# Kernel tuning notes

Hardware: AMD Instinct MI355X
Metric: run time of the kernel (lower is better)

The kernel has to match this reference:

```python
import math
import jax, jax.numpy as jnp
import numpy as np


def _coeffs(alpha, delta, theta, gamma_real, gamma_imag):
    # alpha, delta: (D, N, 1); theta: (D, 1, 1); gamma_*: (D, N)
    D, N, _ = alpha.shape
    scale = math.sqrt(1.0 / float(N))
    th = jax.nn.sigmoid(theta.astype(jnp.float32)) * (2.0 * math.pi / float(N))  # (D,1,1)
    wavelets = jnp.arange(1, N + 1, dtype=jnp.float32).reshape(1, N, 1)
    phi = (wavelets * th)[:, :, 0]                      # (D, N) phase of q
    a = jax.nn.sigmoid(alpha.astype(jnp.float32))[:, :, 0]   # (D, N)
    d = jax.nn.sigmoid(delta.astype(jnp.float32))[:, :, 0]
    p = a                                               # (D, N)
    q_mag = 1.0 - a * d                                 # |q| in (0,1)
    gamma = (gamma_real.astype(jnp.float32) + 1j * gamma_imag.astype(jnp.float32)) * scale
    return p, q_mag, phi, gamma


def reference(x, alpha, delta, theta, gamma_real, gamma_imag, omega):
    # x: (B, D, L). FFT path (hx=None, compute_last_state=False).
    B, D, L = x.shape
    p, q_mag, phi, gamma = _coeffs(alpha, delta, theta, gamma_real, gamma_imag)
    gp = gamma * p.astype(jnp.complex64)                # (D, N) complex
    radius = jnp.minimum(q_mag, 1.0)                    # clamp(max=1.0)
    j = jnp.arange(L, dtype=jnp.float32)                # (L,)
    # q^j = radius^j * exp(i*phi*j); take real part of sum_n gp * q^j directly
    decay = jnp.exp(jnp.log(radius)[:, :, None] * j)    # (D, N, L)
    ang = phi[:, :, None] * j                           # (D, N, L)
    kernel_real = (jnp.einsum('dn,dnl->dl', jnp.real(gp), decay * jnp.cos(ang))
                   - jnp.einsum('dn,dnl->dl', jnp.imag(gp), decay * jnp.sin(ang)))  # (D, L)
    fft_len = 1 << int(2 * L - 1).bit_length()
    X = jnp.fft.rfft(x.astype(jnp.float32), n=fft_len, axis=-1)     # (B, D, F)
    K = jnp.fft.rfft(kernel_real, n=fft_len, axis=-1)               # (D, F)
    y = jnp.fft.irfft(X * K[None], n=fft_len, axis=-1)[..., :L]     # (B, D, L)
    residual = x * omega.astype(x.dtype)[None, :, None]
    return y.astype(x.dtype) + residual


def setup_inputs() -> dict:
    key = jax.random.key(0)
    B, D, L, N = 8, 1024, 2048, 16
    ks = jax.random.split(key, 7)
    x = jax.random.normal(ks[0], (B, D, L), dtype=jnp.float32)
    alpha = 0.2 * jax.random.normal(ks[1], (D, N, 1), dtype=jnp.float32)
    delta = 0.2 * jax.random.normal(ks[2], (D, N, 1), dtype=jnp.float32)
    # theta init: logit of permuted exponentially-spaced freqs (reset_parameters)
    rng = np.random.default_rng(0)
    freqs = np.exp(np.arange(1, D + 1, dtype=np.float32) * (-np.log(D) / D))
    freqs = rng.permutation(freqs)
    freqs = np.clip(freqs, 1e-6, 1.0 - 1e-6)
    theta = jnp.asarray(np.log(freqs / (1.0 - freqs)), dtype=jnp.float32).reshape(D, 1, 1)
    gamma_real = jax.random.normal(ks[3], (D, N), dtype=jnp.float32)
    gamma_imag = 0.1 * jax.random.normal(ks[4], (D, N), dtype=jnp.float32)
    omega = jnp.clip(0.25 * jax.random.normal(ks[5], (D,), dtype=jnp.float32), -1.0, 1.0)
    return {"x": x, "alpha": alpha, "delta": delta, "theta": theta,
            "gamma_real": gamma_real, "gamma_imag": gamma_imag, "omega": omega}
```

## Files before the change

### kernel.cpp

```cpp
#include <hip/hip_runtime.h>
#include <hip/hip_bf16.h>
#include <math.h>


#define Bc 8
#define Dc 1024
#define Lc 2048
#define FRAG_STRIDE 6144
#define SCANW_OFF (Dc * FRAG_STRIDE)
#define ECS 18

typedef _Float16 f16x8 __attribute__((ext_vector_type(8)));
typedef __fp16 h16x2 __attribute__((ext_vector_type(2)));
typedef float f32x4 __attribute__((ext_vector_type(4)));

__device__ inline uint pkh(float a, float b) {
    h16x2 p = __builtin_amdgcn_cvt_pkrtz(a, b);
    union { h16x2 v; uint u; } c; c.v = p;
    return c.u;
}

__device__ inline float2 upk(uint u) {
    union { uint v; __fp16 h[2]; } p; p.v = u;
    return make_float2((float)p.h[0], (float)p.h[1]);
}

__device__ inline f16x8 cvt8(float4 a, float4 b) {
    union { h16x2 h[4]; f16x8 v; } r;
    r.h[0] = __builtin_amdgcn_cvt_pkrtz(a.x, a.y);
    r.h[1] = __builtin_amdgcn_cvt_pkrtz(a.z, a.w);
    r.h[2] = __builtin_amdgcn_cvt_pkrtz(b.x, b.y);
    r.h[3] = __builtin_amdgcn_cvt_pkrtz(b.z, b.w);
    return r.v;
}

__global__ __launch_bounds__(512) void prep_kernel(const float* __restrict__ alpha,
        const float* __restrict__ delta, const float* __restrict__ theta,
        const float* __restrict__ gamma_r, const float* __restrict__ gamma_i,
        const float* __restrict__ omega, char* __restrict__ ws) {
    __shared__ float qpr[16 * 33];
    __shared__ float qpi[16 * 33];
    __shared__ float gprs[16], gpis[16], kap[33];
    const int tid = threadIdx.x;
    const int d = blockIdx.x;

    {
        int n = tid >> 5;
        int j = (tid & 31) + 1;
        int idx = d * 16 + n;
        float a  = 1.f / (1.f + __expf(-alpha[idx]));
        float dl = 1.f / (1.f + __expf(-delta[idx]));
        float th = (1.f / (1.f + __expf(-theta[d]))) * (6.283185307179586f / 16.f);
        float phi = (float)(n + 1) * th;
        float radius = fminf(1.f - a * dl, 1.f);
        float rj = __expf((float)j * __logf(radius));
        float sn, cs; __sincosf((float)j * phi, &sn, &cs);
        qpr[n * 33 + j] = rj * cs;
        qpi[n * 33 + j] = rj * sn;
        if (j == 1) {
            qpr[n * 33] = 1.f; qpi[n * 33] = 0.f;
            gprs[n] = gamma_r[idx] * 0.25f * a;
            gpis[n] = gamma_i[idx] * 0.25f * a;
        }
    }
    __syncthreads();
    if (tid < 33) {
        float s = 0.f;
        #pragma unroll
        for (int n = 0; n < 16; ++n)
            s += gprs[n] * qpr[n * 33 + tid] - gpis[n] * qpi[n * 33 + tid];
        if (tid == 0) s += omega[d];
        kap[tid] = s;
    }
    __syncthreads();
    if (tid < 384) {
        int mat = tid >> 7;
        int sub = tid & 127;
        int rt = sub >> 6, ll = sub & 63;
        int row = rt * 16 + (ll & 15);
        int kb = 8 * (ll >> 4);
        union { _Float16 h[8]; f16x8 v; } fr;
        if (mat == 0) {
            #pragma unroll
            for (int j = 0; j < 8; ++j) {
                int dlt = row - (kb + j);
                fr.h[j] = (_Float16)((dlt >= 0) ? kap[dlt] : 0.f);
            }
        } else if (mat == 1) {
            #pragma unroll
            for (int j = 0; j < 8; ++j) {
                int k = kb + j, n = k >> 1;
                float qr_ = qpr[n * 33 + row + 1], qi_ = qpi[n * 33 + row + 1];
                float gr = gprs[n], gi = gpis[n];
                fr.h[j] = (_Float16)((k & 1) ? -(gr * qi_ + gi * qr_)
                                             : (gr * qr_ - gi * qi_));
            }
        } else {
            int n = row >> 1, im = row & 1;
            #pragma unroll
            for (int j = 0; j < 8; ++j) {
                int mm = kb + j;
                fr.h[j] = (_Float16)(im ? qpi[n * 33 + 31 - mm] : qpr[n * 33 + 31 - mm]);
            }
        }
        *(f16x8*)(ws + (size_t)d * FRAG_STRIDE + mat * 2048 + (rt * 64 + ll) * 16) = fr.v;
    } else if (tid < 400) {
        int n = tid - 384;
        float2* sw = (float2*)(ws + SCANW_OFF);
        sw[d * 16 + n] = make_float2(qpr[n * 33 + 32], qpi[n * 33 + 32]);
    }
}

__global__ __launch_bounds__(512) void ema_main(const float* __restrict__ x,
        const char* __restrict__ ws, float* __restrict__ out) {
    __shared__ uint ECall[8 * 64 * ECS];
    const int tid = threadIdx.x;
    const int w = tid >> 6;
    const int l = tid & 63;
    const int d = blockIdx.x;
    uint* EC = ECall + w * (64 * ECS);
    const int g = l >> 4;
    const int m = l & 15;
    const size_t rowoff = ((size_t)w * Dc + d) * Lc;
    const float4* xr4 = (const float4*)(x + rowoff);
    const f16x8* fr = (const f16x8*)(ws + (size_t)d * FRAG_STRIDE);

    f16x8 xf0, xf1, xf2, xf3;
    {
        const int base = m * 8 + 2 * g;
        float4 a0 = xr4[base],       b0 = xr4[base + 1];
        float4 a1 = xr4[base + 128], b1 = xr4[base + 129];
        float4 a2 = xr4[base + 256], b2 = xr4[base + 257];
        float4 a3 = xr4[base + 384], b3 = xr4[base + 385];
        xf0 = cvt8(a0, b0); xf1 = cvt8(a1, b1);
        xf2 = cvt8(a2, b2); xf3 = cvt8(a3, b3);
    }

    {
        f16x8 va0 = fr[256 + l], va1 = fr[320 + l];
        #define EMFMA(VA, RT, TC, XF) { \
            f32x4 acc = {0.f, 0.f, 0.f, 0.f}; \
            acc = __builtin_amdgcn_mfma_f32_16x16x32_f16(VA, XF, acc, 0, 0, 0); \
            uint2 u; u.x = pkh(acc[0], acc[1]); u.y = pkh(acc[2], acc[3]); \
            *(uint2*)&EC[(TC * 16 + m) * ECS + 8 * RT + 2 * g] = u; }
        EMFMA(va0, 0, 0, xf0) EMFMA(va0, 0, 1, xf1)
        EMFMA(va0, 0, 2, xf2) EMFMA(va0, 0, 3, xf3)
        EMFMA(va1, 1, 0, xf0) EMFMA(va1, 1, 1, xf1)
        EMFMA(va1, 1, 2, xf2) EMFMA(va1, 1, 3, xf3)
        #undef EMFMA
    }

    float w1r[4], w1i[4];
    {
        const float2* sw = (const float2*)(ws + SCANW_OFF + (size_t)d * 128);
        #pragma unroll
        for (int j = 0; j < 4; ++j) {
            float2 t = sw[4 * g + j];
            w1r[j] = t.x; w1i[j] = t.y;
        }
    }
    f16x8 ta0 = fr[l],       ta1 = fr[64 + l];
    f16x8 ga0 = fr[128 + l], ga1 = fr[192 + l];

    __builtin_amdgcn_wave_barrier();

    float4* or4 = (float4*)(out + rowoff);

    #pragma unroll
    for (int tc = 0; tc < 4; ++tc) {
        f16x8 xf = (tc == 0) ? xf0 : (tc == 1) ? xf1 : (tc == 2) ? xf2 : xf3;
        float cr_[4] = {0.f, 0.f, 0.f, 0.f};
        float ci_[4] = {0.f, 0.f, 0.f, 0.f};
        float kr[4] = {1.f, 1.f, 1.f, 1.f};
        float ki[4] = {0.f, 0.f, 0.f, 0.f};
        #pragma unroll
        for (int k = 1; k <= 4; ++k) {
            int c2 = tc * 16 + m - k;
            int cc = (c2 < 0) ? 0 : c2;
            uint2 e0 = *(const uint2*)&EC[cc * ECS + 4 * g];
            uint2 e1 = *(const uint2*)&EC[cc * ECS + 4 * g + 2];
            if (c2 >= 0) {
                float2 aa[4] = { upk(e0.x), upk(e0.y), upk(e1.x), upk(e1.y) };
                #pragma unroll
                for (int j = 0; j < 4; ++j) {
                    cr_[j] = fmaf(kr[j], aa[j].x, fmaf(-ki[j], aa[j].y, cr_[j]));
                    ci_[j] = fmaf(kr[j], aa[j].y, fmaf( ki[j], aa[j].x, ci_[j]));
                }
            }
            if (k < 4) {
                #pragma unroll
                for (int j = 0; j < 4; ++j) {
                    float t2 = fmaf(kr[j], w1r[j], -(ki[j] * w1i[j]));
                    ki[j] = fmaf(kr[j], w1i[j], ki[j] * w1r[j]);
                    kr[j] = t2;
                }
            }
        }
        union { h16x2 h[4]; f16x8 v; } cb;
        #pragma unroll
        for (int j = 0; j < 4; ++j)
            cb.h[j] = __builtin_amdgcn_cvt_pkrtz(cr_[j], ci_[j]);
        f32x4 y0 = {0.f, 0.f, 0.f, 0.f}, y1 = {0.f, 0.f, 0.f, 0.f};
        y0 = __builtin_amdgcn_mfma_f32_16x16x32_f16(ta0, xf,   y0, 0, 0, 0);
        y0 = __builtin_amdgcn_mfma_f32_16x16x32_f16(ga0, cb.v, y0, 0, 0, 0);
        y1 = __builtin_amdgcn_mfma_f32_16x16x32_f16(ta1, xf,   y1, 0, 0, 0);
        y1 = __builtin_amdgcn_mfma_f32_16x16x32_f16(ga1, cb.v, y1, 0, 0, 0);
        float4 o0, o1;
        o0.x = y0[0]; o0.y = y0[1]; o0.z = y0[2]; o0.w = y0[3];
        o1.x = y1[0]; o1.y = y1[1]; o1.z = y1[2]; o1.w = y1[3];
        or4[(tc * 16 + m) * 8 + g]     = o0;
        or4[(tc * 16 + m) * 8 + 4 + g] = o1;
    }
}

extern "C" void kernel_launch(void* const* d_in, const int* in_sizes, int n_in,
                              void* d_out, int out_size, void* d_ws, size_t ws_size,
                              hipStream_t stream) {
    const float* x       = (const float*)d_in[0];
    const float* alpha   = (const float*)d_in[1];
    const float* delta   = (const float*)d_in[2];
    const float* theta   = (const float*)d_in[3];
    const float* gamma_r = (const float*)d_in[4];
    const float* gamma_i = (const float*)d_in[5];
    const float* omega   = (const float*)d_in[6];
    float* out = (float*)d_out;
    char* ws = (char*)d_ws;

    prep_kernel<<<Dc, 512, 0, stream>>>(alpha, delta, theta,
                                        gamma_r, gamma_i, omega, ws);
    ema_main<<<Dc, 512, 0, stream>>>(x, ws, out);
}
```

Measured before the change: 33.49 us.

## Fuse coefficient prep into main EMA kernel using shared-memory fragments

Merges the prep kernel into the main kernel. Each block now computes its own MFMA coefficient fragments and scan weights in LDS instead of writing them to global workspace and reading them back. The x loads are issued before the prep math so their latency overlaps with it. This removes one kernel launch and the global workspace round trip, at the cost of extra block-level barriers and prep work done inside the main kernel, which may lower occupancy or lengthen each block.

```diff
diff --git a/kernel.cpp b/kernel.cpp
--- a/kernel.cpp
+++ b/kernel.cpp
@@ -6,9 +6,8 @@
 #define Bc 8
 #define Dc 1024
 #define Lc 2048
-#define FRAG_STRIDE 6144
-#define SCANW_OFF (Dc * FRAG_STRIDE)
 #define ECS 18
+#define TABW (16 * 33)
 
 typedef _Float16 f16x8 __attribute__((ext_vector_type(8)));
 typedef __fp16 h16x2 __attribute__((ext_vector_type(2)));
@@ -34,15 +33,34 @@
     return r.v;
 }
 
-__global__ __launch_bounds__(512) void prep_kernel(const float* __restrict__ alpha,
-        const float* __restrict__ delta, const float* __restrict__ theta,
-        const float* __restrict__ gamma_r, const float* __restrict__ gamma_i,
-        const float* __restrict__ omega, char* __restrict__ ws) {
-    __shared__ float qpr[16 * 33];
-    __shared__ float qpi[16 * 33];
-    __shared__ float gprs[16], gpis[16], kap[33];
+__global__ __launch_bounds__(512) void ema_fused(const float* __restrict__ x,
+        const float* __restrict__ alpha, const float* __restrict__ delta,
+        const float* __restrict__ theta, const float* __restrict__ gamma_r,
+        const float* __restrict__ gamma_i, const float* __restrict__ omega,
+        float* __restrict__ out) {
+    __shared__ uint ECall[8 * 64 * ECS];
+    __shared__ __align__(16) _Float16 fragH[384 * 8];
+    __shared__ float kap[33], gprs[16], gpis[16];
+    __shared__ float2 scanw[16];
+
     const int tid = threadIdx.x;
     const int d = blockIdx.x;
+    const int w = tid >> 6;
+    const int l = tid & 63;
+    const int g = l >> 4;
+    const int m = l & 15;
+
+    float* qpr = (float*)ECall;
+    float* qpi = qpr + TABW;
+    const f16x8* frag = (const f16x8*)fragH;
+
+    const size_t rowoff = ((size_t)w * Dc + d) * Lc;
+    const float4* xr4 = (const float4*)(x + rowoff);
+    const int base = m * 8 + 2 * g;
+    float4 a0 = xr4[base],       b0 = xr4[base + 1];
+    float4 a1 = xr4[base + 128], b1 = xr4[base + 129];
+    float4 a2 = xr4[base + 256], b2 = xr4[base + 257];
+    float4 a3 = xr4[base + 384], b3 = xr4[base + 385];
 
     {
         int n = tid >> 5;
@@ -55,15 +73,18 @@
         float radius = fminf(1.f - a * dl, 1.f);
         float rj = __expf((float)j * __logf(radius));
         float sn, cs; __sincosf((float)j * phi, &sn, &cs);
-        qpr[n * 33 + j] = rj * cs;
-        qpi[n * 33 + j] = rj * sn;
+        float pr = rj * cs, pi = rj * sn;
+        qpr[n * 33 + j] = pr;
+        qpi[n * 33 + j] = pi;
         if (j == 1) {
             qpr[n * 33] = 1.f; qpi[n * 33] = 0.f;
             gprs[n] = gamma_r[idx] * 0.25f * a;
             gpis[n] = gamma_i[idx] * 0.25f * a;
         }
+        if (j == 32) scanw[n] = make_float2(pr, pi);
     }
     __syncthreads();
+
     if (tid < 33) {
         float s = 0.f;
         #pragma unroll
@@ -73,18 +94,19 @@
         kap[tid] = s;
     }
     __syncthreads();
+
     if (tid < 384) {
         int mat = tid >> 7;
         int sub = tid & 127;
         int rt = sub >> 6, ll = sub & 63;
         int row = rt * 16 + (ll & 15);
         int kb = 8 * (ll >> 4);
-        union { _Float16 h[8]; f16x8 v; } fr;
+        union { _Float16 h[8]; f16x8 v; } fv;
         if (mat == 0) {
             #pragma unroll
             for (int j = 0; j < 8; ++j) {
                 int dlt = row - (kb + j);
-                fr.h[j] = (_Float16)((dlt >= 0) ? kap[dlt] : 0.f);
+                fv.h[j] = (_Float16)((dlt >= 0) ? kap[dlt] : 0.f);
             }
         } else if (mat == 1) {
             #pragma unroll
@@ -92,7 +114,7 @@
                 int k = kb + j, n = k >> 1;
                 float qr_ = qpr[n * 33 + row + 1], qi_ = qpi[n * 33 + row + 1];
                 float gr = gprs[n], gi = gpis[n];
-                fr.h[j] = (_Float16)((k & 1) ? -(gr * qi_ + gi * qr_)
+                fv.h[j] = (_Float16)((k & 1) ? -(gr * qi_ + gi * qr_)
                                              : (gr * qr_ - gi * qi_));
             }
         } else {
@@ -100,44 +122,20 @@
             #pragma unroll
             for (int j = 0; j < 8; ++j) {
                 int mm = kb + j;
-                fr.h[j] = (_Float16)(im ? qpi[n * 33 + 31 - mm] : qpr[n * 33 + 31 - mm]);
+                fv.h[j] = (_Float16)(im ? qpi[n * 33 + 31 - mm] : qpr[n * 33 + 31 - mm]);
             }
         }
-        *(f16x8*)(ws + (size_t)d * FRAG_STRIDE + mat * 2048 + (rt * 64 + ll) * 16) = fr.v;
-    } else if (tid < 400) {
-        int n = tid - 384;
-        float2* sw = (float2*)(ws + SCANW_OFF);
-        sw[d * 16 + n] = make_float2(qpr[n * 33 + 32], qpi[n * 33 + 32]);
-    }
-}
-
-__global__ __launch_bounds__(512) void ema_main(const float* __restrict__ x,
-        const char* __restrict__ ws, float* __restrict__ out) {
-    __shared__ uint ECall[8 * 64 * ECS];
-    const int tid = threadIdx.x;
-    const int w = tid >> 6;
-    const int l = tid & 63;
-    const int d = blockIdx.x;
+        *(f16x8*)&fragH[(mat * 128 + rt * 64 + ll) * 8] = fv.v;
+    }
+    __syncthreads();
+
     uint* EC = ECall + w * (64 * ECS);
-    const int g = l >> 4;
-    const int m = l & 15;
-    const size_t rowoff = ((size_t)w * Dc + d) * Lc;
-    const float4* xr4 = (const float4*)(x + rowoff);
-    const f16x8* fr = (const f16x8*)(ws + (size_t)d * FRAG_STRIDE);
-
-    f16x8 xf0, xf1, xf2, xf3;
+
+    f16x8 xf0 = cvt8(a0, b0), xf1 = cvt8(a1, b1);
+    f16x8 xf2 = cvt8(a2, b2), xf3 = cvt8(a3, b3);
+
     {
-        const int base = m * 8 + 2 * g;
-        float4 a0 = xr4[base],       b0 = xr4[base + 1];
-        float4 a1 = xr4[base + 128], b1 = xr4[base + 129];
-        float4 a2 = xr4[base + 256], b2 = xr4[base + 257];
-        float4 a3 = xr4[base + 384], b3 = xr4[base + 385];
-        xf0 = cvt8(a0, b0); xf1 = cvt8(a1, b1);
-        xf2 = cvt8(a2, b2); xf3 = cvt8(a3, b3);
-    }
-
-    {
-        f16x8 va0 = fr[256 + l], va1 = fr[320 + l];
+        f16x8 va0 = frag[256 + l], va1 = frag[320 + l];
         #define EMFMA(VA, RT, TC, XF) { \
             f32x4 acc = {0.f, 0.f, 0.f, 0.f}; \
             acc = __builtin_amdgcn_mfma_f32_16x16x32_f16(VA, XF, acc, 0, 0, 0); \
@@ -151,16 +149,13 @@
     }
 
     float w1r[4], w1i[4];
-    {
-        const float2* sw = (const float2*)(ws + SCANW_OFF + (size_t)d * 128);
-        #pragma unroll
-        for (int j = 0; j < 4; ++j) {
-            float2 t = sw[4 * g + j];
-            w1r[j] = t.x; w1i[j] = t.y;
-        }
-    }
-    f16x8 ta0 = fr[l],       ta1 = fr[64 + l];
-    f16x8 ga0 = fr[128 + l], ga1 = fr[192 + l];
+    #pragma unroll
+    for (int j = 0; j < 4; ++j) {
+        float2 t = scanw[4 * g + j];
+        w1r[j] = t.x; w1i[j] = t.y;
+    }
+    f16x8 ta0 = frag[l],       ta1 = frag[64 + l];
+    f16x8 ga0 = frag[128 + l], ga1 = frag[192 + l];
 
     __builtin_amdgcn_wave_barrier();
 
@@ -224,9 +219,7 @@
     const float* gamma_i = (const float*)d_in[5];
     const float* omega   = (const float*)d_in[6];
     float* out = (float*)d_out;
-    char* ws = (char*)d_ws;
-
-    prep_kernel<<<Dc, 512, 0, stream>>>(alpha, delta, theta,
-                                        gamma_r, gamma_i, omega, ws);
-    ema_main<<<Dc, 512, 0, stream>>>(x, ws, out);
-}
+
+    ema_fused<<<Dc, 512, 0, stream>>>(x, alpha, delta, theta,
+                                      gamma_r, gamma_i, omega, out);
+}
```

Result: faster. 31.35 us (-6.4%).
